# Performance work log

Measured on AMD Instinct MI355X. Metric: run time of the kernel, lower is better.

The kernel has to match this reference:

```python
import jax, jax.numpy as jnp
import numpy as np
from jax import lax

R = 1          # box-filter radius
EPS = 1e-06    # regularizer


def boxfilter(z, r=R):
    """ReplicationPad2d(r) + depthwise (groups=C) mean conv with kernel (2r+1)^2."""
    k = 2 * r + 1
    c = z.shape[1]
    zp = jnp.pad(z, ((0, 0), (0, 0), (r, r), (r, r)), mode='edge')  # replication pad
    w = jnp.full((c, 1, k, k), 1.0 / (k * k), dtype=z.dtype)        # [O, I/g, kh, kw]
    return lax.conv_general_dilated(zp, w, window_strides=(1, 1), padding='VALID',
                                    feature_group_count=c)


def setup_inputs() -> dict:
    key = jax.random.key(0)
    kx, ky = jax.random.split(key)
    shape = (8, 3, 1024, 1024)
    # image-valued inputs in [0, 255), matching the final clamp range
    x = jax.random.uniform(kx, shape, jnp.float32, 0.0, 255.0)
    y = jax.random.uniform(ky, shape, jnp.float32, 0.0, 255.0)
    return {"x": x, "y": y}


def reference(x, y):
    mean_x = boxfilter(x)
    mean_y = boxfilter(y)
    cov_xy = boxfilter(x * y) - mean_x * mean_y
    var_x = boxfilter(x * x) - mean_x * mean_x
    A = cov_xy / (var_x + EPS)
    b = mean_y - A * mean_x
    res = boxfilter(A) * x + boxfilter(b)
    # torch: res.int() truncates toward zero, clamp(0,255), back to float
    return jnp.clip(jnp.trunc(res), 0.0, 255.0)
```

## Files before the change

kernel.cpp:

```cpp
#include <hip/hip_runtime.h>


typedef float f4 __attribute__((ext_vector_type(4)));

#define TH 32
#define OWPB 248

__global__ __launch_bounds__(256, 4) void gf_kernel(
    const float* __restrict__ xg, const float* __restrict__ yg,
    float* __restrict__ outg, int H, int W) {
  const int lane = threadIdx.x;
  const int img = blockIdx.z;
  const size_t ibase = (size_t)img * H * W;
  const float* __restrict__ xi = xg + ibase;
  const float* __restrict__ yi = yg + ibase;
  float* __restrict__ oi = outg + ibase;

  int tx0 = blockIdx.x * OWPB;
  const int skipb = tx0;
  if (tx0 > W - OWPB) tx0 = W - OWPB;
  const int ty0 = (blockIdx.y * 4 + threadIdx.y) * TH;

  const int c0 = tx0 - 4 + 4 * lane;
  const bool inb = (c0 >= 0) && (c0 <= W - 4);
  const int cbc = (c0 < 0) ? 0 : (W - 1);
  const bool wok = (lane >= 1) && (lane <= 62) && (c0 >= skipb);
  const bool leftE = (tx0 == 0);
  const bool rightE = (tx0 + OWPB >= W);
  const float inv9 = 1.0f / 9.0f;

  f4 xr0, xr1, xr2, yr0, yr1, yr2, xpf, ypf;
  f4 hA0, hA1, hA2, hA3, hB0, hB1, hB2, hB3;
  int nextr;

  auto ldrow = [&](int r, f4& xv, f4& yv) {
    const float* xr = xi + (size_t)r * W;
    const float* yr = yi + (size_t)r * W;
    if (inb) {
      xv = *(const f4*)(xr + c0);
      yv = *(const f4*)(yr + c0);
    } else {
      float a = xr[cbc], b = yr[cbc];
      xv = (f4)(a);
      yv = (f4)(b);
    }
  };

  auto hsum3 = [&](f4 v) {
    float vl = __shfl_up(v[3], 1);
    float vr = __shfl_down(v[0], 1);
    float a01 = v[0] + v[1], a12 = v[1] + v[2], a23 = v[2] + v[3];
    f4 s;
    s[0] = vl + a01;
    s[1] = a01 + v[2];
    s[2] = a12 + v[3];
    s[3] = a23 + vr;
    return s;
  };

  auto emit_row = [&](int ly, f4 xv) {
    f4 SA = hA1 + hA2 + hA3;
    f4 SB = hB1 + hB2 + hB3;
    f4 st;
#pragma unroll
    for (int j = 0; j < 4; ++j) {
      float res = (SA[j] * xv[j] + SB[j]) * inv9;
      float t = truncf(res);
      st[j] = fminf(fmaxf(t, 0.0f), 255.0f);
    }
    if (wok) {
      int gr = ty0 + ly - 2;
      __builtin_nontemporal_store(st, (f4*)(oi + (size_t)gr * W + c0));
    }
  };

  auto dup_hist = [&]() {
    hA0 = hA1; hA1 = hA2; hA2 = hA3;
    hB0 = hB1; hB1 = hB2; hB2 = hB3;
  };

  auto step_adv = [&](int ly, bool doemit, bool dopf) {
    xr0 = xr1; xr1 = xr2; xr2 = xpf;
    yr0 = yr1; yr1 = yr2; yr2 = ypf;
    if (dopf) {
      ldrow(nextr, xpf, ypf);
      nextr = min(nextr + 1, H - 1);
    }
    f4 vx = xr0 + xr1 + xr2;
    f4 vy = yr0 + yr1 + yr2;
    f4 vxy = xr0 * yr0 + xr1 * yr1 + xr2 * yr2;
    f4 vxx = xr0 * xr0 + xr1 * xr1 + xr2 * xr2;
    f4 Sx = hsum3(vx), Sy = hsum3(vy), Sxy = hsum3(vxy), Sxx = hsum3(vxx);
    f4 A, B;
#pragma unroll
    for (int j = 0; j < 4; ++j) {
      float num = 9.0f * Sxy[j] - Sx[j] * Sy[j];
      float den = 9.0f * Sxx[j] - Sx[j] * Sx[j] + 8.1e-05f;
      float rd;
      asm("v_rcp_f32 %0, %1" : "=v"(rd) : "v"(den));
      float a = num * rd;
      A[j] = a;
      B[j] = Sy[j] * inv9 - a * (Sx[j] * inv9);
    }
    if (leftE) {
      float ta = __shfl_down(A[0], 1), tb = __shfl_down(B[0], 1);
      if (lane == 0) { A[3] = ta; B[3] = tb; }
    }
    if (rightE) {
      float ta = __shfl_up(A[3], 1), tb = __shfl_up(B[3], 1);
      if (lane == 63) { A[0] = ta; B[0] = tb; }
    }
    f4 hAn = hsum3(A), hBn = hsum3(B);
    hA0 = hA1; hA1 = hA2; hA2 = hA3; hA3 = hAn;
    hB0 = hB1; hB1 = hB2; hB2 = hB3; hB3 = hBn;
    if (doemit) emit_row(ly, xr0);
  };

  {
    int cy0 = max(ty0 - 1, 0);
    int ra = max(cy0 - 1, 0);
    ldrow(ra, xr1, yr1);
    ldrow(cy0, xr2, yr2);
    nextr = min(cy0 + 1, H - 1);
    ldrow(nextr, xpf, ypf);
    nextr = min(nextr + 1, H - 1);
  }
  hA0 = hA1 = hA2 = hA3 = (f4)(0.0f);
  hB0 = hB1 = hB2 = hB3 = (f4)(0.0f);

  step_adv(0, false, true);
  if (ty0 == 0) dup_hist();
  else step_adv(1, false, true);
#pragma unroll 4
  for (int ly = 2; ly <= TH; ++ly) step_adv(ly, true, true);
  if (ty0 == H - TH) {
    dup_hist();
    emit_row(TH + 1, xr1);
  } else {
    step_adv(TH + 1, true, false);
  }
}

extern "C" void kernel_launch(void* const* d_in, const int* in_sizes, int n_in,
                              void* d_out, int out_size, void* d_ws, size_t ws_size,
                              hipStream_t stream) {
  const float* x = (const float*)d_in[0];
  const float* y = (const float*)d_in[1];
  float* out = (float*)d_out;
  const int H = 1024, W = 1024;
  const int imgs = in_sizes[0] / (H * W);
  dim3 block(64, 4, 1);
  dim3 grid((W + OWPB - 1) / OWPB, H / (TH * 4), imgs);
  gf_kernel<<<grid, block, 0, stream>>>(x, y, out, H, W);
}
```

Measured before the change: 266.8 us.

## Replace cross-lane shuffles with per-thread halo loads and shrink row tile

Each thread now loads its own 2-column halo on both sides of its 4-wide chunk, so the horizontal 3-tap sums for the statistics and for A/B need no wavefront shuffles. Blocks no longer overlap by halo columns, which removes the wasted edge lanes and masked stores of the 248-wide tiling. The row tile per wave is halved to 16 and the occupancy hint is dropped, giving more blocks but more redundant vertical halo rows per block. The trade-off is extra overlapping loads and redundant A/B computation (6 instead of 4 per thread) in exchange for removing shuffles and the idle lanes.

```diff
diff --git a/kernel.cpp b/kernel.cpp
--- a/kernel.cpp
+++ b/kernel.cpp
@@ -2,11 +2,14 @@
 
 
 typedef float f4 __attribute__((ext_vector_type(4)));
+typedef float f2 __attribute__((ext_vector_type(2)));
 
-#define TH 32
-#define OWPB 248
+#define TH 16
+#define OW 256
 
-__global__ __launch_bounds__(256, 4) void gf_kernel(
+struct Row { f2 xl; f4 xm; f2 xr; f2 yl; f4 ym; f2 yr; };
+
+__global__ __launch_bounds__(256) void gf_kernel(
     const float* __restrict__ xg, const float* __restrict__ yg,
     float* __restrict__ outg, int H, int W) {
   const int lane = threadIdx.x;
@@ -16,46 +19,30 @@
   const float* __restrict__ yi = yg + ibase;
   float* __restrict__ oi = outg + ibase;
 
-  int tx0 = blockIdx.x * OWPB;
-  const int skipb = tx0;
-  if (tx0 > W - OWPB) tx0 = W - OWPB;
+  const int tx0 = blockIdx.x * OW;
   const int ty0 = (blockIdx.y * 4 + threadIdx.y) * TH;
-
-  const int c0 = tx0 - 4 + 4 * lane;
-  const bool inb = (c0 >= 0) && (c0 <= W - 4);
-  const int cbc = (c0 < 0) ? 0 : (W - 1);
-  const bool wok = (lane >= 1) && (lane <= 62) && (c0 >= skipb);
-  const bool leftE = (tx0 == 0);
-  const bool rightE = (tx0 + OWPB >= W);
+  const int o0 = tx0 + 4 * lane;
+  const bool fixl = (o0 == 0);
+  const bool fixr = (o0 == W - 4);
+  const int olo = fixl ? 0 : (o0 - 2);
+  const int ohi = fixr ? (W - 2) : (o0 + 4);
   const float inv9 = 1.0f / 9.0f;
 
-  f4 xr0, xr1, xr2, yr0, yr1, yr2, xpf, ypf;
+  Row r0, r1, r2, pf;
   f4 hA0, hA1, hA2, hA3, hB0, hB1, hB2, hB3;
   int nextr;
 
-  auto ldrow = [&](int r, f4& xv, f4& yv) {
-    const float* xr = xi + (size_t)r * W;
-    const float* yr = yi + (size_t)r * W;
-    if (inb) {
-      xv = *(const f4*)(xr + c0);
-      yv = *(const f4*)(yr + c0);
-    } else {
-      float a = xr[cbc], b = yr[cbc];
-      xv = (f4)(a);
-      yv = (f4)(b);
-    }
-  };
-
-  auto hsum3 = [&](f4 v) {
-    float vl = __shfl_up(v[3], 1);
-    float vr = __shfl_down(v[0], 1);
-    float a01 = v[0] + v[1], a12 = v[1] + v[2], a23 = v[2] + v[3];
-    f4 s;
-    s[0] = vl + a01;
-    s[1] = a01 + v[2];
-    s[2] = a12 + v[3];
-    s[3] = a23 + vr;
-    return s;
+  auto ldrow = [&](int rr, Row& R) {
+    const float* xr = xi + (size_t)rr * W;
+    const float* yr = yi + (size_t)rr * W;
+    R.xm = *(const f4*)(xr + o0);
+    R.xl = *(const f2*)(xr + olo);
+    R.xr = *(const f2*)(xr + ohi);
+    R.ym = *(const f4*)(yr + o0);
+    R.yl = *(const f2*)(yr + olo);
+    R.yr = *(const f2*)(yr + ohi);
+    if (fixl) { R.xl[1] = R.xl[0]; R.yl[1] = R.yl[0]; }
+    if (fixr) { R.xr[0] = R.xr[1]; R.yr[0] = R.yr[1]; }
   };
 
   auto emit_row = [&](int ly, f4 xv) {
@@ -68,10 +55,8 @@
       float t = truncf(res);
       st[j] = fminf(fmaxf(t, 0.0f), 255.0f);
     }
-    if (wok) {
-      int gr = ty0 + ly - 2;
-      __builtin_nontemporal_store(st, (f4*)(oi + (size_t)gr * W + c0));
-    }
+    int gr = ty0 + ly - 2;
+    __builtin_nontemporal_store(st, (f4*)(oi + (size_t)gr * W + o0));
   };
 
   auto dup_hist = [&]() {
@@ -80,49 +65,62 @@
   };
 
   auto step_adv = [&](int ly, bool doemit, bool dopf) {
-    xr0 = xr1; xr1 = xr2; xr2 = xpf;
-    yr0 = yr1; yr1 = yr2; yr2 = ypf;
+    r0 = r1; r1 = r2; r2 = pf;
     if (dopf) {
-      ldrow(nextr, xpf, ypf);
+      ldrow(nextr, pf);
       nextr = min(nextr + 1, H - 1);
     }
-    f4 vx = xr0 + xr1 + xr2;
-    f4 vy = yr0 + yr1 + yr2;
-    f4 vxy = xr0 * yr0 + xr1 * yr1 + xr2 * yr2;
-    f4 vxx = xr0 * xr0 + xr1 * xr1 + xr2 * xr2;
-    f4 Sx = hsum3(vx), Sy = hsum3(vy), Sxy = hsum3(vxy), Sxx = hsum3(vxx);
-    f4 A, B;
+    f2 vxl = r0.xl + r1.xl + r2.xl;
+    f4 vxm = r0.xm + r1.xm + r2.xm;
+    f2 vxr = r0.xr + r1.xr + r2.xr;
+    f2 vyl = r0.yl + r1.yl + r2.yl;
+    f4 vym = r0.ym + r1.ym + r2.ym;
+    f2 vyr = r0.yr + r1.yr + r2.yr;
+    f2 vxyl = r0.xl * r0.yl + r1.xl * r1.yl + r2.xl * r2.yl;
+    f4 vxym = r0.xm * r0.ym + r1.xm * r1.ym + r2.xm * r2.ym;
+    f2 vxyr = r0.xr * r0.yr + r1.xr * r1.yr + r2.xr * r2.yr;
+    f2 vxxl = r0.xl * r0.xl + r1.xl * r1.xl + r2.xl * r2.xl;
+    f4 vxxm = r0.xm * r0.xm + r1.xm * r1.xm + r2.xm * r2.xm;
+    f2 vxxr = r0.xr * r0.xr + r1.xr * r1.xr + r2.xr * r2.xr;
+    float vx[8]  = {vxl[0],  vxl[1],  vxm[0],  vxm[1],  vxm[2],  vxm[3],  vxr[0],  vxr[1]};
+    float vy[8]  = {vyl[0],  vyl[1],  vym[0],  vym[1],  vym[2],  vym[3],  vyr[0],  vyr[1]};
+    float vxy[8] = {vxyl[0], vxyl[1], vxym[0], vxym[1], vxym[2], vxym[3], vxyr[0], vxyr[1]};
+    float vxx[8] = {vxxl[0], vxxl[1], vxxm[0], vxxm[1], vxxm[2], vxxm[3], vxxr[0], vxxr[1]};
+    float A[6], B[6];
 #pragma unroll
-    for (int j = 0; j < 4; ++j) {
-      float num = 9.0f * Sxy[j] - Sx[j] * Sy[j];
-      float den = 9.0f * Sxx[j] - Sx[j] * Sx[j] + 8.1e-05f;
+    for (int j = 0; j < 6; ++j) {
+      float Sx  = vx[j] + vx[j + 1] + vx[j + 2];
+      float Sy  = vy[j] + vy[j + 1] + vy[j + 2];
+      float Sxy = vxy[j] + vxy[j + 1] + vxy[j + 2];
+      float Sxx = vxx[j] + vxx[j + 1] + vxx[j + 2];
+      float num = 9.0f * Sxy - Sx * Sy;
+      float den = 9.0f * Sxx - Sx * Sx + 8.1e-05f;
       float rd;
       asm("v_rcp_f32 %0, %1" : "=v"(rd) : "v"(den));
       float a = num * rd;
       A[j] = a;
-      B[j] = Sy[j] * inv9 - a * (Sx[j] * inv9);
+      B[j] = Sy * inv9 - a * (Sx * inv9);
     }
-    if (leftE) {
-      float ta = __shfl_down(A[0], 1), tb = __shfl_down(B[0], 1);
-      if (lane == 0) { A[3] = ta; B[3] = tb; }
+    if (fixl) { A[0] = A[1]; B[0] = B[1]; }
+    if (fixr) { A[5] = A[4]; B[5] = B[4]; }
+    f4 hAn, hBn;
+#pragma unroll
+    for (int j = 0; j < 4; ++j) {
+      hAn[j] = A[j] + A[j + 1] + A[j + 2];
+      hBn[j] = B[j] + B[j + 1] + B[j + 2];
     }
-    if (rightE) {
-      float ta = __shfl_up(A[3], 1), tb = __shfl_up(B[3], 1);
-      if (lane == 63) { A[0] = ta; B[0] = tb; }
-    }
-    f4 hAn = hsum3(A), hBn = hsum3(B);
     hA0 = hA1; hA1 = hA2; hA2 = hA3; hA3 = hAn;
     hB0 = hB1; hB1 = hB2; hB2 = hB3; hB3 = hBn;
-    if (doemit) emit_row(ly, xr0);
+    if (doemit) emit_row(ly, r0.xm);
   };
 
   {
     int cy0 = max(ty0 - 1, 0);
     int ra = max(cy0 - 1, 0);
-    ldrow(ra, xr1, yr1);
-    ldrow(cy0, xr2, yr2);
+    ldrow(ra, r1);
+    ldrow(cy0, r2);
     nextr = min(cy0 + 1, H - 1);
-    ldrow(nextr, xpf, ypf);
+    ldrow(nextr, pf);
     nextr = min(nextr + 1, H - 1);
   }
   hA0 = hA1 = hA2 = hA3 = (f4)(0.0f);
@@ -135,7 +133,7 @@
   for (int ly = 2; ly <= TH; ++ly) step_adv(ly, true, true);
   if (ty0 == H - TH) {
     dup_hist();
-    emit_row(TH + 1, xr1);
+    emit_row(TH + 1, r1.xm);
   } else {
     step_adv(TH + 1, true, false);
   }
@@ -150,6 +148,6 @@
   const int H = 1024, W = 1024;
   const int imgs = in_sizes[0] / (H * W);
   dim3 block(64, 4, 1);
-  dim3 grid((W + OWPB - 1) / OWPB, H / (TH * 4), imgs);
+  dim3 grid(W / OW, H / (TH * 4), imgs);
   gf_kernel<<<grid, block, 0, stream>>>(x, y, out, H, W);
 }
```

Result: faster. 248.6 us (-6.8%).
